# Performance work log

Measured on AMD Instinct MI355X. Metric: run time of the kernel, lower is better.

## Reference

```python
import jax, jax.numpy as jnp
import numpy as np

B, T1, T2 = 16, 1024, 1024
K1D, K2D, V1D, V2D, A = 512, 512, 256, 256, 128


def setup_inputs() -> dict:
    key = jax.random.key(0)
    ks = jax.random.split(key, 10)
    inp = {
        "k1": jax.random.normal(ks[0], (B, T1, K1D), dtype=jnp.float32),
        "k2": jax.random.normal(ks[1], (B, T2, K2D), dtype=jnp.float32),
        "v1": jax.random.normal(ks[2], (B, T1, V1D), dtype=jnp.float32),
        "v2": jax.random.normal(ks[3], (B, T2, V2D), dtype=jnp.float32),
        # Linear params (torch nn.Linear: y = x @ W.T + b)
        "W1": jax.random.normal(ks[4], (A, K1D), dtype=jnp.float32) / np.sqrt(K1D),
        "b1": jnp.zeros((A,), dtype=jnp.float32),
        "W2": jax.random.normal(ks[5], (A, K2D), dtype=jnp.float32) / np.sqrt(K2D),
        "b2": jnp.zeros((A,), dtype=jnp.float32),
        # valid lengths in [T/2, T-1] so no softmax row is entirely -inf
        "k1_lengths": jax.random.randint(ks[6], (B,), T1 // 2, T1, dtype=jnp.int32),
        "k2_lengths": jax.random.randint(ks[7], (B,), T2 // 2, T2, dtype=jnp.int32),
    }
    return inp


def reference(k1, k2, v1, v2, W1, b1, W2, b2, k1_lengths, k2_lengths):
    # projections
    q1 = jnp.einsum("bti,ai->bta", k1, W1) + b1  # [B,T1,A]
    q2 = jnp.einsum("bti,ai->bta", k2, W2) + b2  # [B,T2,A]
    # co-attention score [B,T1,T2]
    score = jnp.einsum("bia,bja->bij", q1, q2)
    # faithful mask: torch code adds 1 for rows>=l1 and 1 for cols>=l2,
    # then masks where sum == 1  -> XOR of the two pad conditions.
    row_pad = jnp.arange(T1)[None, :, None] >= k1_lengths[:, None, None]  # [B,T1,1]
    col_pad = jnp.arange(T2)[None, None, :] >= k2_lengths[:, None, None]  # [B,1,T2]
    mask = jnp.logical_xor(row_pad, col_pad)
    score = jnp.where(mask, -jnp.inf, score)
    # dual softmaxes
    w1 = jax.nn.softmax(jnp.swapaxes(score, 1, 2), axis=-1)  # [B,T2,T1]
    w2 = jax.nn.softmax(score, axis=-1)                      # [B,T1,T2]
    o1 = jnp.einsum("bji,bid->bjd", w1, v1)  # [B,T2,V1D]
    o2 = jnp.einsum("bij,bjd->bid", w2, v2)  # [B,T1,V2D]
    # note: the torch module additionally slices w1/w2/score per sample to
    # (l2,l1)/(l1,l2) ragged views; with fixed shapes we return the full
    # tensors (the valid region matches; slicing is a zero-copy view in torch).
    return (o1, o2, w1, w2, score)
```

## Files before the change

### kernel.cpp

```cpp
#include <hip/hip_runtime.h>
#include <math.h>

namespace {
constexpr int TT   = 1024;
constexpr int AD   = 128;
constexpr int KDIM = 512;
constexpr int VDIM = 256;
constexpr int NB   = 16;
constexpr size_t T2T = (size_t)TT * TT;
constexpr size_t BT  = (size_t)NB * TT;
}

#define MASK_VAL (-1.0e30f)


typedef __bf16 bf16x8 __attribute__((ext_vector_type(8)));
typedef float  f32x4  __attribute__((ext_vector_type(4)));

__device__ __forceinline__ unsigned short bf16_rne(float x) {
    unsigned int u = __builtin_bit_cast(unsigned int, x);
    u += 0x7fffu + ((u >> 16) & 1u);
    return (unsigned short)(u >> 16);
}
__device__ __forceinline__ float bf16f(unsigned short h) {
    return __builtin_bit_cast(float, ((unsigned int)h) << 16);
}
__device__ __forceinline__ void split2(float x, unsigned short& h, unsigned short& l) {
    h = bf16_rne(x);
    l = bf16_rne(x - bf16f(h));
}
__device__ __forceinline__ bf16x8 as_bf16x8(uint4 u) {
    return __builtin_bit_cast(bf16x8, u);
}

__global__ __launch_bounds__(256) void prep_fused_kernel(
    const float* __restrict__ v1, const float* __restrict__ v2,
    unsigned short* __restrict__ vth, unsigned short* __restrict__ vtl,
    const float* __restrict__ k1, const float* __restrict__ W1, const float* __restrict__ bias1,
    const float* __restrict__ k2, const float* __restrict__ W2, const float* __restrict__ bias2,
    unsigned short* __restrict__ q1h, unsigned short* __restrict__ q1l,
    unsigned short* __restrict__ q2h, unsigned short* __restrict__ q2l)
{
    __shared__ alignas(16) char smem[40960];
    const int tid = threadIdx.x;

    if (blockIdx.x < 1024) {
        const int pid   = blockIdx.x;
        const int which = pid >> 9;
        const int rest  = pid & 511;
        const int b     = rest & 15;
        const int k0    = (rest >> 4) * 32;
        const float* vb = (which ? v1 : v2) + (size_t)b * TT * VDIM;
        float (*ls)[257] = (float(*)[257])smem;

#pragma unroll
        for (int rep = 0; rep < 8; ++rep) {
            int idx = tid + rep * 256;
            int k  = idx >> 6;
            int n4 = (idx & 63) * 4;
            float4 x = *(const float4*)(vb + (size_t)(k0 + k) * VDIM + n4);
            ls[k][n4 + 0] = x.x;
            ls[k][n4 + 1] = x.y;
            ls[k][n4 + 2] = x.z;
            ls[k][n4 + 3] = x.w;
        }
        __syncthreads();

        const size_t pbase = ((size_t)(which * NB + b)) * VDIM * TT;
        const int kb = k0 >> 5;
#pragma unroll
        for (int rep = 0; rep < 4; ++rep) {
            int idx = tid + rep * 256;
            int n  = idx >> 2;
            int sg = (idx & 3) * 8;
            unsigned short h[8], l[8];
#pragma unroll
            for (int j = 0; j < 8; ++j) {
                float x = ls[sg + j][n];
                split2(x, h[j], l[j]);
            }
            uint4 H, L;
            H.x = (unsigned)h[0] | ((unsigned)h[1] << 16);
            H.y = (unsigned)h[2] | ((unsigned)h[3] << 16);
            H.z = (unsigned)h[4] | ((unsigned)h[5] << 16);
            H.w = (unsigned)h[6] | ((unsigned)h[7] << 16);
            L.x = (unsigned)l[0] | ((unsigned)l[1] << 16);
            L.y = (unsigned)l[2] | ((unsigned)l[3] << 16);
            L.z = (unsigned)l[4] | ((unsigned)l[5] << 16);
            L.w = (unsigned)l[6] | ((unsigned)l[7] << 16);
            size_t off = pbase + (size_t)(((n >> 4) * 32 + kb) * 512)
                               + (size_t)(((sg >> 3) * 16 + (n & 15)) * 8);
            *(uint4*)(vth + off) = H;
            *(uint4*)(vtl + off) = L;
        }
        return;
    }

    const int qid  = blockIdx.x - 1024;
    const int proj = qid >> 7;
    const int m0   = (qid & 127) * 128;
    const float* __restrict__ K    = proj ? k2 : k1;
    const float* __restrict__ W    = proj ? W2 : W1;
    const float* __restrict__ bias = proj ? bias2 : bias1;
    unsigned short* __restrict__ qh = proj ? q2h : q1h;
    unsigned short* __restrict__ ql = proj ? q2l : q1l;

    unsigned short* akh = (unsigned short*)smem;
    unsigned short* akl = akh + 128 * 40;
    unsigned short* bwh = akl + 128 * 40;
    unsigned short* bwl = bwh + 128 * 40;

    const int lane = tid & 63;
    const int wv   = tid >> 6;
    const int wm = wv >> 1, wn = wv & 1;
    const int la = lane & 15, kg = lane >> 4;

    f32x4 acc[4][4];
#pragma unroll
    for (int m = 0; m < 4; ++m)
#pragma unroll
        for (int n = 0; n < 4; ++n) acc[m][n] = (f32x4){0.f, 0.f, 0.f, 0.f};

    for (int k0 = 0; k0 < KDIM; k0 += 32) {
#pragma unroll
        for (int rep = 0; rep < 4; ++rep) {
            int idx = tid + rep * 256;
            int row = idx >> 3, c4 = (idx & 7) * 4;
            float4 x = *(const float4*)(K + (size_t)(m0 + row) * KDIM + k0 + c4);
            ushort4 H, L;
            split2(x.x, H.x, L.x);
            split2(x.y, H.y, L.y);
            split2(x.z, H.z, L.z);
            split2(x.w, H.w, L.w);
            *(ushort4*)&akh[row * 40 + c4] = H;
            *(ushort4*)&akl[row * 40 + c4] = L;
        }
#pragma unroll
        for (int rep = 0; rep < 4; ++rep) {
            int idx = tid + rep * 256;
            int row = idx >> 3, c4 = (idx & 7) * 4;
            float4 x = *(const float4*)(W + (size_t)row * KDIM + k0 + c4);
            ushort4 H, L;
            split2(x.x, H.x, L.x);
            split2(x.y, H.y, L.y);
            split2(x.z, H.z, L.z);
            split2(x.w, H.w, L.w);
            *(ushort4*)&bwh[row * 40 + c4] = H;
            *(ushort4*)&bwl[row * 40 + c4] = L;
        }
        __syncthreads();

        bf16x8 ah[4], al[4], bh[4], bl[4];
#pragma unroll
        for (int m = 0; m < 4; ++m) {
            int r = wm * 64 + m * 16 + la;
            ah[m] = *(const bf16x8*)&akh[r * 40 + kg * 8];
            al[m] = *(const bf16x8*)&akl[r * 40 + kg * 8];
        }
#pragma unroll
        for (int n = 0; n < 4; ++n) {
            int c = wn * 64 + n * 16 + la;
            bh[n] = *(const bf16x8*)&bwh[c * 40 + kg * 8];
            bl[n] = *(const bf16x8*)&bwl[c * 40 + kg * 8];
        }
        __builtin_amdgcn_s_setprio(1);
#pragma unroll
        for (int m = 0; m < 4; ++m)
#pragma unroll
            for (int n = 0; n < 4; ++n) {
                acc[m][n] = __builtin_amdgcn_mfma_f32_16x16x32_bf16(ah[m], bh[n], acc[m][n], 0, 0, 0);
                acc[m][n] = __builtin_amdgcn_mfma_f32_16x16x32_bf16(ah[m], bl[n], acc[m][n], 0, 0, 0);
                acc[m][n] = __builtin_amdgcn_mfma_f32_16x16x32_bf16(al[m], bh[n], acc[m][n], 0, 0, 0);
            }
        __builtin_amdgcn_s_setprio(0);
        __syncthreads();
    }

#pragma unroll
    for (int n = 0; n < 4; ++n) {
        int col = wn * 64 + n * 16 + la;
        float bv = bias[col];
        int kb  = col >> 5;
        int kgs = (col >> 3) & 3;
        int e   = col & 7;
#pragma unroll
        for (int m = 0; m < 4; ++m) {
            int rb = (m0 >> 4) + wm * 4 + m;
            size_t blk = (size_t)(rb * 4 + kb) * 512;
#pragma unroll
            for (int r = 0; r < 4; ++r) {
                int las = kg * 4 + r;
                size_t off = blk + (size_t)(kgs * 16 + las) * 8 + e;
                unsigned short h, l;
                split2(acc[m][n][r] + bv, h, l);
                qh[off] = h;
                ql[off] = l;
            }
        }
    }
}

__global__ __launch_bounds__(256) void score_mfma_stats_kernel(
    const unsigned short* __restrict__ q1h, const unsigned short* __restrict__ q1l,
    const unsigned short* __restrict__ q2h, const unsigned short* __restrict__ q2l,
    const int* __restrict__ len1, const int* __restrict__ len2,
    float* __restrict__ score,
    float* __restrict__ prm, float* __restrict__ prs,
    float* __restrict__ pcm, float* __restrict__ pcs)
{
    const int b  = blockIdx.x;
    const int mt = blockIdx.y >> 3, nt = blockIdx.y & 7;
    const int m0 = mt * 128, n0 = nt * 128;
    const size_t qoff = (size_t)b * TT * AD;

    __shared__ float red_m[2][128];
    __shared__ float red_s[2][128];

    const int tid  = threadIdx.x;
    const int lane = tid & 63;
    const int wv   = tid >> 6;
    const int wm = wv >> 1, wn = wv & 1;
    const int la = lane & 15, kg = lane >> 4;
    const int slot8 = (kg * 16 + la) * 8;

    f32x4 acc[4][4];
#pragma unroll
    for (int m = 0; m < 4; ++m)
#pragma unroll
        for (int n = 0; n < 4; ++n) acc[m][n] = (f32x4){0.f, 0.f, 0.f, 0.f};

#pragma unroll
    for (int kb = 0; kb < 4; ++kb) {
        bf16x8 ah[4], al[4], bh[4], bl[4];
#pragma unroll
        for (int m = 0; m < 4; ++m) {
            int rb = (m0 >> 4) + wm * 4 + m;
            size_t off = qoff + (size_t)((rb * 4 + kb) * 512) + slot8;
            ah[m] = as_bf16x8(*(const uint4*)(q1h + off));
            al[m] = as_bf16x8(*(const uint4*)(q1l + off));
        }
#pragma unroll
        for (int n = 0; n < 4; ++n) {
            int rb = (n0 >> 4) + wn * 4 + n;
            size_t off = qoff + (size_t)((rb * 4 + kb) * 512) + slot8;
            bh[n] = as_bf16x8(*(const uint4*)(q2h + off));
            bl[n] = as_bf16x8(*(const uint4*)(q2l + off));
        }
        __builtin_amdgcn_s_setprio(1);
#pragma unroll
        for (int m = 0; m < 4; ++m)
#pragma unroll
            for (int n = 0; n < 4; ++n) {
                acc[m][n] = __builtin_amdgcn_mfma_f32_16x16x32_bf16(ah[m], bh[n], acc[m][n], 0, 0, 0);
                acc[m][n] = __builtin_amdgcn_mfma_f32_16x16x32_bf16(ah[m], bl[n], acc[m][n], 0, 0, 0);
                acc[m][n] = __builtin_amdgcn_mfma_f32_16x16x32_bf16(al[m], bh[n], acc[m][n], 0, 0, 0);
            }
        __builtin_amdgcn_s_setprio(0);
    }

    const int l1v = len1[b];
    const int l2v = len2[b];

#pragma unroll
    for (int m = 0; m < 4; ++m)
#pragma unroll
        for (int r = 0; r < 4; ++r) {
            int row = m0 + wm * 64 + m * 16 + kg * 4 + r;
            bool rp = row >= l1v;
#pragma unroll
            for (int n = 0; n < 4; ++n) {
                int col = n0 + wn * 64 + n * 16 + la;
                bool cp = col >= l2v;
                if (rp != cp) acc[m][n][r] = MASK_VAL;
            }
        }
    float* sb = score + (size_t)b * T2T;
#pragma unroll
    for (int m = 0; m < 4; ++m)
#pragma unroll
        for (int r = 0; r < 4; ++r) {
            int row = m0 + wm * 64 + m * 16 + kg * 4 + r;
#pragma unroll
            for (int n = 0; n < 4; ++n) {
                int col = n0 + wn * 64 + n * 16 + la;
                sb[(size_t)row * TT + col] = acc[m][n][r];
            }
        }

#pragma unroll
    for (int m = 0; m < 4; ++m)
#pragma unroll
        for (int r = 0; r < 4; ++r) {
            float mr = fmaxf(fmaxf(acc[m][0][r], acc[m][1][r]),
                             fmaxf(acc[m][2][r], acc[m][3][r]));
#pragma unroll
            for (int off = 1; off <= 8; off <<= 1) mr = fmaxf(mr, __shfl_xor(mr, off));
            float sr = __expf(acc[m][0][r] - mr) + __expf(acc[m][1][r] - mr) +
                       __expf(acc[m][2][r] - mr) + __expf(acc[m][3][r] - mr);
#pragma unroll
            for (int off = 1; off <= 8; off <<= 1) sr += __shfl_xor(sr, off);
            if (la == 0) {
                int rloc = wm * 64 + m * 16 + kg * 4 + r;
                red_m[wn][rloc] = mr;
                red_s[wn][rloc] = sr;
            }
        }
    __syncthreads();
    if (tid < 128) {
        float ma = red_m[0][tid], mb2 = red_m[1][tid];
        float mm = fmaxf(ma, mb2);
        float ss = red_s[0][tid] * __expf(ma - mm) + red_s[1][tid] * __expf(mb2 - mm);
        prm[(size_t)nt * BT + (size_t)b * TT + m0 + tid] = mm;
        prs[(size_t)nt * BT + (size_t)b * TT + m0 + tid] = ss;
    }
    __syncthreads();

#pragma unroll
    for (int n = 0; n < 4; ++n) {
        float mc = MASK_VAL;
#pragma unroll
        for (int m = 0; m < 4; ++m)
#pragma unroll
            for (int r = 0; r < 4; ++r) mc = fmaxf(mc, acc[m][n][r]);
#pragma unroll
        for (int off = 16; off <= 32; off <<= 1) mc = fmaxf(mc, __shfl_xor(mc, off));
        float sc = 0.f;
#pragma unroll
        for (int m = 0; m < 4; ++m)
#pragma unroll
            for (int r = 0; r < 4; ++r) sc += __expf(acc[m][n][r] - mc);
#pragma unroll
        for (int off = 16; off <= 32; off <<= 1) sc += __shfl_xor(sc, off);
        if (kg == 0) {
            int cloc = wn * 64 + n * 16 + la;
            red_m[wm][cloc] = mc;
            red_s[wm][cloc] = sc;
        }
    }
    __syncthreads();
    if (tid < 128) {
        float ma = red_m[0][tid], mb2 = red_m[1][tid];
        float mm = fmaxf(ma, mb2);
        float ss = red_s[0][tid] * __expf(ma - mm) + red_s[1][tid] * __expf(mb2 - mm);
        pcm[(size_t)mt * BT + (size_t)b * TT + n0 + tid] = mm;
        pcs[(size_t)mt * BT + (size_t)b * TT + n0 + tid] = ss;
    }
}

__global__ __launch_bounds__(512) void ogemm_fused_kernel(
    const float* __restrict__ score,
    const float* __restrict__ prm, const float* __restrict__ prs,
    const float* __restrict__ pcm, const float* __restrict__ pcs,
    const unsigned short* __restrict__ vth, const unsigned short* __restrict__ vtl,
    float* __restrict__ w2, float* __restrict__ w1,
    float* __restrict__ o2, float* __restrict__ o1)
{
    const int b     = blockIdx.x;
    const int m0    = blockIdx.y * 128;
    const int which = blockIdx.z;
    const size_t vbase = ((size_t)(which * NB + b)) * VDIM * TT;

    const float* __restrict__ sb = score + (size_t)b * T2T;
    float* __restrict__ wout = (which ? w1 : w2) + (size_t)b * T2T;
    float* __restrict__ ob   = (which ? o1 : o2) + (size_t)b * TT * VDIM;

    __shared__ alignas(16) unsigned short awh[2][128 * 40];
    __shared__ alignas(16) unsigned short awl[2][128 * 40];
    __shared__ float st[128][33];
    __shared__ float sm_s[128], si_s[128];

    const int tid  = threadIdx.x;
    const int lane = tid & 63;
    const int wv   = tid >> 6;
    const int wm   = wv >> 2;
    const int wn   = wv & 3;
    const int la = lane & 15, kg = lane >> 4;
    const int slot8 = (kg * 16 + la) * 8;

    const int r_row0 = tid >> 3,          r_c4_0 = (tid & 7) * 4;
    const int r_row1 = (tid + 512) >> 3,  r_c4_1 = ((tid + 512) & 7) * 4;
    const int c_ip0 = tid >> 5,           c_c4_0 = (tid & 31) * 4;
    const int c_ip1 = (tid + 512) >> 5,   c_c4_1 = ((tid + 512) & 31) * 4;

    if (tid < 128) {
        const float* pm = which ? pcm : prm;
        const float* ps = which ? pcs : prs;
        size_t base = (size_t)b * TT + m0 + tid;
        float nm = MASK_VAL;
#pragma unroll
        for (int c = 0; c < 8; ++c) nm = fmaxf(nm, pm[(size_t)c * BT + base]);
        float s = 0.f;
#pragma unroll
        for (int c = 0; c < 8; ++c)
            s += ps[(size_t)c * BT + base] * __expf(pm[(size_t)c * BT + base] - nm);
        sm_s[tid] = nm;
        si_s[tid] = 1.f / s;
    }
    __syncthreads();

    f32x4 acc[4][4];
#pragma unroll
    for (int m = 0; m < 4; ++m)
#pragma unroll
        for (int n = 0; n < 4; ++n) acc[m][n] = (f32x4){0.f, 0.f, 0.f, 0.f};

    float4 aA0, aA1;
    auto issueA = [&](int k0) {
        if (which == 0) {
            aA0 = *(const float4*)(sb + (size_t)(m0 + r_row0) * TT + k0 + r_c4_0);
            aA1 = *(const float4*)(sb + (size_t)(m0 + r_row1) * TT + k0 + r_c4_1);
        } else {
            aA0 = *(const float4*)(sb + (size_t)(k0 + c_ip0) * TT + m0 + c_c4_0);
            aA1 = *(const float4*)(sb + (size_t)(k0 + c_ip1) * TT + m0 + c_c4_1);
        }
    };

    issueA(0);

    int cur = 0;
    for (int k0 = 0; k0 < TT; k0 += 32, cur ^= 1) {
        unsigned short* AWH = &awh[cur][0];
        unsigned short* AWL = &awl[cur][0];
        const int kb = k0 >> 5;

        if (which == 0) {
#pragma unroll
            for (int rep = 0; rep < 2; ++rep) {
                float4 x = rep ? aA1 : aA0;
                int row = rep ? r_row1 : r_row0;
                int c4  = rep ? r_c4_1 : r_c4_0;
                float mm = sm_s[row], ii = si_s[row];
                f32x4 wv4;
                wv4[0] = __expf(x.x - mm) * ii;
                wv4[1] = __expf(x.y - mm) * ii;
                wv4[2] = __expf(x.z - mm) * ii;
                wv4[3] = __expf(x.w - mm) * ii;
                __builtin_nontemporal_store(wv4, (f32x4*)(wout + (size_t)(m0 + row) * TT + k0 + c4));
                ushort4 H, L;
                split2(wv4[0], H.x, L.x);
                split2(wv4[1], H.y, L.y);
                split2(wv4[2], H.z, L.z);
                split2(wv4[3], H.w, L.w);
                *(ushort4*)&AWH[row * 40 + c4] = H;
                *(ushort4*)&AWL[row * 40 + c4] = L;
            }
            if (k0 + 32 < TT) issueA(k0 + 32);
            __syncthreads();
        } else {
            {
                float4 x = aA0;
                st[c_c4_0 + 0][c_ip0] = __expf(x.x - sm_s[c_c4_0 + 0]) * si_s[c_c4_0 + 0];
                st[c_c4_0 + 1][c_ip0] = __expf(x.y - sm_s[c_c4_0 + 1]) * si_s[c_c4_0 + 1];
                st[c_c4_0 + 2][c_ip0] = __expf(x.z - sm_s[c_c4_0 + 2]) * si_s[c_c4_0 + 2];
                st[c_c4_0 + 3][c_ip0] = __expf(x.w - sm_s[c_c4_0 + 3]) * si_s[c_c4_0 + 3];
                x = aA1;
                st[c_c4_1 + 0][c_ip1] = __expf(x.x - sm_s[c_c4_1 + 0]) * si_s[c_c4_1 + 0];
                st[c_c4_1 + 1][c_ip1] = __expf(x.y - sm_s[c_c4_1 + 1]) * si_s[c_c4_1 + 1];
                st[c_c4_1 + 2][c_ip1] = __expf(x.z - sm_s[c_c4_1 + 2]) * si_s[c_c4_1 + 2];
                st[c_c4_1 + 3][c_ip1] = __expf(x.w - sm_s[c_c4_1 + 3]) * si_s[c_c4_1 + 3];
            }
            if (k0 + 32 < TT) issueA(k0 + 32);
            __syncthreads();
#pragma unroll
            for (int rep = 0; rep < 2; ++rep) {
                int idx = tid + rep * 512;
                int j = idx >> 3, i4 = (idx & 7) * 4;
                f32x4 wv4;
                wv4[0] = st[j][i4 + 0];
                wv4[1] = st[j][i4 + 1];
                wv4[2] = st[j][i4 + 2];
                wv4[3] = st[j][i4 + 3];
                __builtin_nontemporal_store(wv4, (f32x4*)(wout + (size_t)(m0 + j) * TT + k0 + i4));
                ushort4 H, L;
                split2(wv4[0], H.x, L.x);
                split2(wv4[1], H.y, L.y);
                split2(wv4[2], H.z, L.z);
                split2(wv4[3], H.w, L.w);
                *(ushort4*)&AWH[j * 40 + i4] = H;
                *(ushort4*)&AWL[j * 40 + i4] = L;
            }
            __syncthreads();
        }

        bf16x8 ah[4], al[4], bh[4], bl[4];
#pragma unroll
        for (int n = 0; n < 4; ++n) {
            size_t off = vbase + (size_t)(((wn * 4 + n) * 32 + kb) * 512) + slot8;
            bh[n] = as_bf16x8(*(const uint4*)(vth + off));
            bl[n] = as_bf16x8(*(const uint4*)(vtl + off));
        }
#pragma unroll
        for (int m = 0; m < 4; ++m) {
            int r = wm * 64 + m * 16 + la;
            ah[m] = *(const bf16x8*)&AWH[r * 40 + kg * 8];
            al[m] = *(const bf16x8*)&AWL[r * 40 + kg * 8];
        }
        __builtin_amdgcn_s_setprio(1);
#pragma unroll
        for (int m = 0; m < 4; ++m)
#pragma unroll
            for (int n = 0; n < 4; ++n) {
                acc[m][n] = __builtin_amdgcn_mfma_f32_16x16x32_bf16(ah[m], bh[n], acc[m][n], 0, 0, 0);
                acc[m][n] = __builtin_amdgcn_mfma_f32_16x16x32_bf16(ah[m], bl[n], acc[m][n], 0, 0, 0);
                acc[m][n] = __builtin_amdgcn_mfma_f32_16x16x32_bf16(al[m], bh[n], acc[m][n], 0, 0, 0);
            }
        __builtin_amdgcn_s_setprio(0);
    }

#pragma unroll
    for (int m = 0; m < 4; ++m)
#pragma unroll
        for (int r = 0; r < 4; ++r) {
            int row = m0 + wm * 64 + m * 16 + kg * 4 + r;
#pragma unroll
            for (int n = 0; n < 4; ++n) {
                int col = wn * 64 + n * 16 + la;
                __builtin_nontemporal_store(acc[m][n][r], ob + (size_t)row * VDIM + col);
            }
        }
}

extern "C" void kernel_launch(void* const* d_in, const int* in_sizes, int n_in,
                              void* d_out, int out_size, void* d_ws, size_t ws_size,
                              hipStream_t stream) {
    const float* k1 = (const float*)d_in[0];
    const float* k2 = (const float*)d_in[1];
    const float* v1 = (const float*)d_in[2];
    const float* v2 = (const float*)d_in[3];
    const float* W1 = (const float*)d_in[4];
    const float* b1 = (const float*)d_in[5];
    const float* W2 = (const float*)d_in[6];
    const float* b2 = (const float*)d_in[7];
    const int* len1 = (const int*)d_in[8];
    const int* len2 = (const int*)d_in[9];

    float* out = (float*)d_out;
    float* o1    = out;
    float* o2    = out + (size_t)NB * TT * VDIM;
    float* w1    = out + (size_t)2 * NB * TT * VDIM;
    float* w2    = w1 + (size_t)NB * T2T;
    float* score = w2 + (size_t)NB * T2T;

    float* ws   = (float*)d_ws;
    float* prm  = ws;
    float* prs  = prm + 8 * BT;
    float* pcm  = prs + 8 * BT;
    float* pcs  = pcm + 8 * BT;
    unsigned short* q1h = (unsigned short*)(pcs + 8 * BT);
    unsigned short* q1l = q1h + BT * AD;
    unsigned short* q2h = q1l + BT * AD;
    unsigned short* q2l = q2h + BT * AD;
    unsigned short* vth = q2l + BT * AD;
    unsigned short* vtl = vth + (size_t)32 * VDIM * TT;

    prep_fused_kernel<<<dim3(1280), 256, 0, stream>>>(v1, v2, vth, vtl,
                                                      k1, W1, b1, k2, W2, b2,
                                                      q1h, q1l, q2h, q2l);
    score_mfma_stats_kernel<<<dim3(NB, 64), 256, 0, stream>>>(q1h, q1l, q2h, q2l,
                                                              len1, len2, score,
                                                              prm, prs, pcm, pcs);
    ogemm_fused_kernel<<<dim3(NB, TT / 128, 2), 512, 0, stream>>>(score, prm, prs, pcm, pcs,
                                                                  vth, vtl, w2, w1, o2, o1);
}
```

Before: 162.2 us.

## Stage V operand through double-buffered LDS with register prefetch

The packed V hi/lo planes are now stored in a plain [n][T] transposed layout instead of a fragment-swizzled layout. The weight-times-V kernel loads each 32-wide K slice cooperatively into registers one iteration ahead, writes it into double-buffered LDS, and reads MFMA B fragments from LDS. Previously each wave read its B fragments directly from global memory. The aim is to hide global latency through prefetch and to share V tiles across the waves in the M dimension. The cost is about 80KB of extra LDS, which may reduce occupancy.

```diff
diff --git a/kernel.cpp b/kernel.cpp
--- a/kernel.cpp
+++ b/kernel.cpp
@@ -67,7 +67,6 @@
         __syncthreads();
 
         const size_t pbase = ((size_t)(which * NB + b)) * VDIM * TT;
-        const int kb = k0 >> 5;
 #pragma unroll
         for (int rep = 0; rep < 4; ++rep) {
             int idx = tid + rep * 256;
@@ -88,8 +87,7 @@
             L.y = (unsigned)l[2] | ((unsigned)l[3] << 16);
             L.z = (unsigned)l[4] | ((unsigned)l[5] << 16);
             L.w = (unsigned)l[6] | ((unsigned)l[7] << 16);
-            size_t off = pbase + (size_t)(((n >> 4) * 32 + kb) * 512)
-                               + (size_t)(((sg >> 3) * 16 + (n & 15)) * 8);
+            size_t off = pbase + (size_t)n * TT + k0 + sg;
             *(uint4*)(vth + off) = H;
             *(uint4*)(vtl + off) = L;
         }
@@ -366,6 +364,8 @@
 
     __shared__ alignas(16) unsigned short awh[2][128 * 40];
     __shared__ alignas(16) unsigned short awl[2][128 * 40];
+    __shared__ alignas(16) unsigned short bvh[2][256 * 40];
+    __shared__ alignas(16) unsigned short bvl[2][256 * 40];
     __shared__ float st[128][33];
     __shared__ float sm_s[128], si_s[128];
 
@@ -375,12 +375,13 @@
     const int wm   = wv >> 2;
     const int wn   = wv & 3;
     const int la = lane & 15, kg = lane >> 4;
-    const int slot8 = (kg * 16 + la) * 8;
 
     const int r_row0 = tid >> 3,          r_c4_0 = (tid & 7) * 4;
     const int r_row1 = (tid + 512) >> 3,  r_c4_1 = ((tid + 512) & 7) * 4;
     const int c_ip0 = tid >> 5,           c_c4_0 = (tid & 31) * 4;
     const int c_ip1 = (tid + 512) >> 5,   c_c4_1 = ((tid + 512) & 31) * 4;
+    const int b_n0 = tid >> 2,            b_sg = (tid & 3) * 8;
+    const int b_n1 = b_n0 + 128;
 
     if (tid < 128) {
         const float* pm = which ? pcm : prm;
@@ -405,6 +406,8 @@
         for (int n = 0; n < 4; ++n) acc[m][n] = (f32x4){0.f, 0.f, 0.f, 0.f};
 
     float4 aA0, aA1;
+    uint4  bh0, bh1, bl0, bl1;
+
     auto issueA = [&](int k0) {
         if (which == 0) {
             aA0 = *(const float4*)(sb + (size_t)(m0 + r_row0) * TT + k0 + r_c4_0);
@@ -414,14 +417,30 @@
             aA1 = *(const float4*)(sb + (size_t)(k0 + c_ip1) * TT + m0 + c_c4_1);
         }
     };
+    auto issueB = [&](int k0) {
+        size_t off0 = vbase + (size_t)b_n0 * TT + k0 + b_sg;
+        size_t off1 = vbase + (size_t)b_n1 * TT + k0 + b_sg;
+        bh0 = *(const uint4*)(vth + off0);
+        bh1 = *(const uint4*)(vth + off1);
+        bl0 = *(const uint4*)(vtl + off0);
+        bl1 = *(const uint4*)(vtl + off1);
+    };
 
     issueA(0);
+    issueB(0);
 
     int cur = 0;
     for (int k0 = 0; k0 < TT; k0 += 32, cur ^= 1) {
         unsigned short* AWH = &awh[cur][0];
         unsigned short* AWL = &awl[cur][0];
-        const int kb = k0 >> 5;
+        unsigned short* BVH = &bvh[cur][0];
+        unsigned short* BVL = &bvl[cur][0];
+
+        *(uint4*)&BVH[b_n0 * 40 + b_sg] = bh0;
+        *(uint4*)&BVH[b_n1 * 40 + b_sg] = bh1;
+        *(uint4*)&BVL[b_n0 * 40 + b_sg] = bl0;
+        *(uint4*)&BVL[b_n1 * 40 + b_sg] = bl1;
+        if (k0 + 32 < TT) issueB(k0 + 32);
 
         if (which == 0) {
 #pragma unroll
@@ -484,16 +503,16 @@
 
         bf16x8 ah[4], al[4], bh[4], bl[4];
 #pragma unroll
-        for (int n = 0; n < 4; ++n) {
-            size_t off = vbase + (size_t)(((wn * 4 + n) * 32 + kb) * 512) + slot8;
-            bh[n] = as_bf16x8(*(const uint4*)(vth + off));
-            bl[n] = as_bf16x8(*(const uint4*)(vtl + off));
-        }
-#pragma unroll
         for (int m = 0; m < 4; ++m) {
             int r = wm * 64 + m * 16 + la;
             ah[m] = *(const bf16x8*)&AWH[r * 40 + kg * 8];
             al[m] = *(const bf16x8*)&AWL[r * 40 + kg * 8];
+        }
+#pragma unroll
+        for (int n = 0; n < 4; ++n) {
+            int c = wn * 64 + n * 16 + la;
+            bh[n] = *(const bf16x8*)&BVH[c * 40 + kg * 8];
+            bl[n] = *(const bf16x8*)&BVL[c * 40 + kg * 8];
         }
         __builtin_amdgcn_s_setprio(1);
 #pragma unroll
```

New measurement: 167.8 us. 3.4% more time.
